# Kernel tuning notes

Measured on AMD Instinct MI355X. Metric: run time of the kernel, lower is better.

The kernel has to match this reference:

```python
import jax, jax.numpy as jnp
import numpy as np

B, LQ, LK, E, H, TOPK = 8, 512, 2048, 512, 8, 20
HD = E // H  # head dim = 64


def setup_inputs() -> dict:
    key = jax.random.key(0)
    ks = jax.random.split(key, 8)
    s = 1.0 / np.sqrt(E)
    return {
        "q": jax.random.normal(ks[0], (B, LQ, E), jnp.float32),
        "k": jax.random.normal(ks[1], (B, LK, E), jnp.float32),
        "v": jax.random.normal(ks[2], (B, LK, E), jnp.float32),
        "Wq": jax.random.normal(ks[3], (E, E), jnp.float32) * s,
        "Wk": jax.random.normal(ks[4], (E, E), jnp.float32) * s,
        "Wv": jax.random.normal(ks[5], (E, E), jnp.float32) * s,
        "Wo": jax.random.normal(ks[6], (E, E), jnp.float32) * s,
        "bo": jnp.zeros((E,), jnp.float32),
    }


def reference(q, k, v, Wq, Wk, Wv, Wo, bo):
    # torch Linear: y = x @ W^T
    def heads(x, W, L):
        return (x @ W.T).reshape(B, L, H, HD).transpose(0, 2, 1, 3)  # [B,H,L,HD]

    query = heads(q, Wq, LQ)
    key_ = heads(k, Wk, LK)
    value = heads(v, Wv, LK)

    scores = jnp.einsum("bhqd,bhkd->bhqk", query, key_) / np.sqrt(HD)
    scores = jax.nn.softmax(scores, axis=-1)  # [B,H,LQ,LK]

    topk_vals, topk_idx = jax.lax.top_k(scores, TOPK)  # [B,H,LQ,K]

    # scatter top-k probs back into a sparse weight matrix (rest zero)
    bi = jnp.arange(B)[:, None, None, None]
    hi = jnp.arange(H)[None, :, None, None]
    qi = jnp.arange(LQ)[None, None, :, None]
    attn = jnp.zeros_like(scores).at[bi, hi, qi, topk_idx].set(topk_vals)

    out = jnp.einsum("bhqk,bhkd->bhqd", attn, value)
    out = out.transpose(0, 2, 1, 3).reshape(B, LQ, E)
    return out @ Wo.T + bo + q
```

## Files before the change

kernel.cpp:

```cpp
#include <hip/hip_runtime.h>
#include <hip/hip_bf16.h>

#define NB 8
#define LQ 512
#define LK 2048
#define EE 512
#define NH 8
#define HD 64
#define NTOPK 20
#define GRP 4

typedef float f4v __attribute__((ext_vector_type(4)));
typedef short s8v __attribute__((ext_vector_type(8)));
typedef __bf16 bfrag __attribute__((ext_vector_type(8)));

__device__ inline short f2bf(float f) {
    union { float f; unsigned u; } x; x.f = f;
    unsigned r = (x.u + 0x7FFFu + ((x.u >> 16) & 1u)) >> 16;
    return (short)r;
}
__device__ inline float bf2f(short s) {
    union { unsigned u; float f; } x;
    x.u = ((unsigned)(unsigned short)s) << 16;
    return x.f;
}

__global__ __launch_bounds__(256) void cvt_all(
    const float* __restrict__ q, const float* __restrict__ k, const float* __restrict__ v,
    const float* __restrict__ wq, const float* __restrict__ wk, const float* __restrict__ wv,
    const float* __restrict__ wo,
    short* __restrict__ qb, short* __restrict__ kb, short* __restrict__ vb,
    short* __restrict__ wqb, short* __restrict__ wkb, short* __restrict__ wvb,
    short* __restrict__ wob)
{
    const float* src; short* dst; int n;
    switch (blockIdx.y) {
        case 0: src = q;  dst = qb;  n = NB * LQ * EE; break;
        case 1: src = k;  dst = kb;  n = NB * LK * EE; break;
        case 2: src = v;  dst = vb;  n = NB * LK * EE; break;
        case 3: src = wq; dst = wqb; n = EE * EE; break;
        case 4: src = wk; dst = wkb; n = EE * EE; break;
        case 5: src = wv; dst = wvb; n = EE * EE; break;
        default: src = wo; dst = wob; n = EE * EE; break;
    }
    const int nv = n >> 3;
    for (int i = blockIdx.x * 256 + threadIdx.x; i < nv; i += gridDim.x * 256) {
        f4v a = *(const f4v*)&src[(size_t)i * 8];
        f4v b = *(const f4v*)&src[(size_t)i * 8 + 4];
        s8v o;
        o[0] = f2bf(a[0]); o[1] = f2bf(a[1]); o[2] = f2bf(a[2]); o[3] = f2bf(a[3]);
        o[4] = f2bf(b[0]); o[5] = f2bf(b[1]); o[6] = f2bf(b[2]); o[7] = f2bf(b[3]);
        *(s8v*)&dst[(size_t)i * 8] = o;
    }
}

template<int MODE>
__global__ __launch_bounds__(256) void gemm_bf16(
    const short* __restrict__ A, const short* __restrict__ W,
    void* __restrict__ C, const float* __restrict__ bias,
    const float* __restrict__ resid)
{
    __shared__ short As[128][72];
    __shared__ short Bs[128][72];
    const int tid  = threadIdx.x;
    const int lane = tid & 63;
    const int wr   = (tid >> 7) & 1;
    const int wc   = (tid >> 6) & 1;
    const size_t bm = (size_t)blockIdx.y * 128;
    const int    bn = blockIdx.x * 128;

    f4v acc[4][4] = {};
    const int lr  = lane & 15;
    const int kg  = (lane >> 4) * 8;
    const int srow = tid >> 3;
    const int sc8  = (tid & 7) * 8;

    for (int ks = 0; ks < EE; ks += 64) {
        #pragma unroll
        for (int i = 0; i < 4; i++) {
            const int row = i * 32 + srow;
            *(s8v*)&As[row][sc8] = *(const s8v*)&A[(bm + row) * EE + ks + sc8];
            *(s8v*)&Bs[row][sc8] = *(const s8v*)&W[(size_t)(bn + row) * EE + ks + sc8];
        }
        __syncthreads();
        #pragma unroll
        for (int kk = 0; kk < 64; kk += 32) {
            bfrag af[4], bf[4];
            #pragma unroll
            for (int mi = 0; mi < 4; mi++)
                af[mi] = *(const bfrag*)&As[wr * 64 + mi * 16 + lr][kk + kg];
            #pragma unroll
            for (int ni = 0; ni < 4; ni++)
                bf[ni] = *(const bfrag*)&Bs[wc * 64 + ni * 16 + lr][kk + kg];
            #pragma unroll
            for (int mi = 0; mi < 4; mi++)
                #pragma unroll
                for (int ni = 0; ni < 4; ni++)
                    acc[mi][ni] = __builtin_amdgcn_mfma_f32_16x16x32_bf16(
                        af[mi], bf[ni], acc[mi][ni], 0, 0, 0);
        }
        __syncthreads();
    }

    const int rj = (lane >> 4) * 4;
    #pragma unroll
    for (int mi = 0; mi < 4; mi++) {
        #pragma unroll
        for (int ni = 0; ni < 4; ni++) {
            const int    col  = bn + wc * 64 + ni * 16 + lr;
            const size_t row0 = bm + wr * 64 + mi * 16 + rj;
            #pragma unroll
            for (int j = 0; j < 4; j++) {
                const float  v   = acc[mi][ni][j];
                const size_t idx = (row0 + j) * EE + col;
                if (MODE == 0) ((short*)C)[idx] = f2bf(v);
                else           ((float*)C)[idx] = v + bias[col] + resid[idx];
            }
        }
    }
}

__global__ __launch_bounds__(256) void score_gemm(
    const short* __restrict__ Qp, const short* __restrict__ Kp,
    short* __restrict__ Sg, int group)
{
    __shared__ short As[128][72];
    __shared__ short Bs[128][72];
    const int tid  = threadIdx.x;
    const int lane = tid & 63;
    const int wr   = (tid >> 7) & 1;
    const int wc   = (tid >> 6) & 1;
    const int z  = blockIdx.z;
    const int h  = z & 7;
    const int b  = group * GRP + (z >> 3);
    const int bm = blockIdx.y * 128;
    const int bn = blockIdx.x * 128;

    const short* Ab = Qp + (size_t)b * LQ * EE + h * HD;
    const short* Bb = Kp + (size_t)b * LK * EE + h * HD;

    #pragma unroll
    for (int i = 0; i < 4; i++) {
        const int row = i * 32 + (tid >> 3);
        const int c8  = (tid & 7) * 8;
        *(s8v*)&As[row][c8] = *(const s8v*)&Ab[(size_t)(bm + row) * EE + c8];
        *(s8v*)&Bs[row][c8] = *(const s8v*)&Bb[(size_t)(bn + row) * EE + c8];
    }
    __syncthreads();

    f4v acc[4][4] = {};
    const int lr = lane & 15;
    const int kg = (lane >> 4) * 8;
    #pragma unroll
    for (int kk = 0; kk < HD; kk += 32) {
        bfrag af[4], bf[4];
        #pragma unroll
        for (int mi = 0; mi < 4; mi++)
            af[mi] = *(const bfrag*)&As[wr * 64 + mi * 16 + lr][kk + kg];
        #pragma unroll
        for (int ni = 0; ni < 4; ni++)
            bf[ni] = *(const bfrag*)&Bs[wc * 64 + ni * 16 + lr][kk + kg];
        #pragma unroll
        for (int mi = 0; mi < 4; mi++)
            #pragma unroll
            for (int ni = 0; ni < 4; ni++)
                acc[mi][ni] = __builtin_amdgcn_mfma_f32_16x16x32_bf16(
                    af[mi], bf[ni], acc[mi][ni], 0, 0, 0);
    }

    short* Sh = Sg + (size_t)z * LQ * LK;
    const int rj = (lane >> 4) * 4;
    #pragma unroll
    for (int mi = 0; mi < 4; mi++) {
        #pragma unroll
        for (int ni = 0; ni < 4; ni++) {
            const int col = bn + wc * 64 + ni * 16 + lr;
            const int r0  = bm + wr * 64 + mi * 16 + rj;
            #pragma unroll
            for (int j = 0; j < 4; j++)
                Sh[(size_t)(r0 + j) * LK + col] = f2bf(acc[mi][ni][j] * 0.125f);
        }
    }
}

__global__ __launch_bounds__(256) void topk_pv(
    const unsigned short* __restrict__ Sg, const short* __restrict__ Vp,
    short* __restrict__ attn, int group)
{
    const int lane = threadIdx.x & 63;
    const int wid  = threadIdx.x >> 6;
    const int r  = blockIdx.x * 4 + wid;
    const int h  = (r >> 9) & 7;
    const int qi = r & 511;
    const int b  = group * GRP + (r >> 12);
    const unsigned short* Srow = Sg + (size_t)r * LK;

    s8v raw[4];
    unsigned key[32];
    const unsigned invl = 2047u - (unsigned)(lane * 8);
    #pragma unroll
    for (int t = 0; t < 4; t++) {
        raw[t] = *(const s8v*)&Srow[t * 512 + lane * 8];
        #pragma unroll
        for (int e = 0; e < 8; e++) {
            const unsigned u = (unsigned short)raw[t][e];
            const unsigned sgn = (unsigned)((int)(u << 16) >> 31);
            const unsigned mono = u ^ (0x8000u | (sgn & 0x7FFFu));
            key[t * 8 + e] = (mono << 11) | (invl - (unsigned)(t * 512 + e));
        }
    }

    unsigned v1 = 0, v2 = 0;
    #pragma unroll
    for (int c = 0; c < 32; c++) {
        const unsigned kc = key[c];
        const unsigned mn = v1 < kc ? v1 : kc;
        v2 = v2 > mn ? v2 : mn;
        v1 = v1 > kc ? v1 : kc;
    }

    unsigned K = v1;
    #pragma unroll
    for (int o = 32; o; o >>= 1) {
        const unsigned ok = __shfl_xor(K, o);
        K = K > ok ? K : ok;
    }
    const unsigned mtop = K >> 11;
    const unsigned mbits = (mtop & 0x8000u) ? (mtop ^ 0x8000u) : (~mtop & 0xFFFFu);
    union { unsigned u; float f; } mu; mu.u = mbits << 16;
    const float M = mu.f;

    float sum = 0.f;
    #pragma unroll
    for (int t = 0; t < 4; t++)
        #pragma unroll
        for (int e = 0; e < 8; e++)
            sum += __expf(bf2f(raw[t][e]) - M);
    #pragma unroll
    for (int o = 32; o; o >>= 1) sum += __shfl_xor(sum, o);
    const float inv = 1.f / sum;

    float oacc = 0.f;
    unsigned rm = 0;
    const short* Vb = Vp + (size_t)b * LK * EE + h * HD + lane;

    #pragma unroll 1
    for (int kk = 0; kk < NTOPK; kk++) {
        const unsigned idx = 2047u - (K & 2047u);
        const unsigned mo  = K >> 11;
        const unsigned sb  = (mo & 0x8000u) ? (mo ^ 0x8000u) : (~mo & 0xFFFFu);
        union { unsigned u; float f; } su; su.u = sb << 16;
        const float p = __expf(su.f - M) * inv;
        oacc += p * bf2f(Vb[(size_t)idx * EE]);

        const bool mine = (v1 == K);
        if (mine) {
            const unsigned slot = ((idx >> 9) << 3) | (idx & 7u);
            rm |= (1u << slot);
            v1 = v2;
            v2 = 0;
        }
        if (__any(v1 == 0u)) {
            if (v1 == 0u) {
                unsigned a1 = 0, a2 = 0;
                #pragma unroll
                for (int c = 0; c < 32; c++) {
                    const unsigned kc = (rm & (1u << c)) ? 0u : key[c];
                    const unsigned mn = a1 < kc ? a1 : kc;
                    a2 = a2 > mn ? a2 : mn;
                    a1 = a1 > kc ? a1 : kc;
                }
                v1 = a1; v2 = a2;
            }
        }
        K = v1;
        #pragma unroll
        for (int o = 32; o; o >>= 1) {
            const unsigned ok = __shfl_xor(K, o);
            K = K > ok ? K : ok;
        }
    }
    attn[((size_t)b * LQ + qi) * EE + h * HD + lane] = f2bf(oacc);
}

extern "C" void kernel_launch(void* const* d_in, const int* in_sizes, int n_in,
                              void* d_out, int out_size, void* d_ws, size_t ws_size,
                              hipStream_t stream)
{
    const float* q  = (const float*)d_in[0];
    const float* k  = (const float*)d_in[1];
    const float* v  = (const float*)d_in[2];
    const float* Wq = (const float*)d_in[3];
    const float* Wk = (const float*)d_in[4];
    const float* Wv = (const float*)d_in[5];
    const float* Wo = (const float*)d_in[6];
    const float* bo = (const float*)d_in[7];

    if (ws_size < ((size_t)160 << 20)) return;

    char*  ws  = (char*)d_ws;
    short* qb  = (short*)(ws);
    short* kb  = (short*)(ws + ((size_t)4   << 20));
    short* vb  = (short*)(ws + ((size_t)20  << 20));
    short* wqb = (short*)(ws + ((size_t)36  << 20));
    short* wkb = (short*)(ws + ((size_t)36  << 20) + (512 << 10));
    short* wvb = (short*)(ws + ((size_t)37  << 20));
    short* wob = (short*)(ws + ((size_t)37  << 20) + (512 << 10));
    short* Qp  = (short*)(ws + ((size_t)38  << 20));
    short* Kp  = (short*)(ws + ((size_t)42  << 20));
    short* Vp  = (short*)(ws + ((size_t)58  << 20));
    short* att = (short*)(ws + ((size_t)74  << 20));
    short* Sg  = (short*)(ws + ((size_t)80  << 20));

    dim3 blk(256);
    cvt_all<<<dim3(512, 7), blk, 0, stream>>>(q, k, v, Wq, Wk, Wv, Wo,
                                              qb, kb, vb, wqb, wkb, wvb, wob);

    gemm_bf16<0><<<dim3(4, 32),  blk, 0, stream>>>(qb, wqb, Qp, nullptr, nullptr);
    gemm_bf16<0><<<dim3(4, 128), blk, 0, stream>>>(kb, wkb, Kp, nullptr, nullptr);
    gemm_bf16<0><<<dim3(4, 128), blk, 0, stream>>>(vb, wvb, Vp, nullptr, nullptr);

    for (int g = 0; g < NB / GRP; g++) {
        score_gemm<<<dim3(LK / 128, LQ / 128, GRP * NH), blk, 0, stream>>>(Qp, Kp, Sg, g);
        topk_pv<<<dim3(GRP * NH * LQ / 4), blk, 0, stream>>>((const unsigned short*)Sg, Vp, att, g);
    }

    gemm_bf16<2><<<dim3(4, 32), blk, 0, stream>>>(att, wob, (float*)d_out, bo, q);
}
```

Before: 316.5 us.

## Process all batches in one launch and decouple top-k selection from V gathers

Makes the score GEMM and top-k kernels cover all 8 batches in a single launch each instead of two groups, which doubles the score buffer in the workspace. Replaces the shuffle-based wave reductions with DPP-based max and sum reductions. Stops storing the 32 per-lane keys in registers and recomputes them from the raw bf16 scores when a lane needs a refill, which lowers register pressure. The top-k loop now writes the selected probabilities and indices to shared memory, and the V gathers run afterwards in a fully unrolled loop, so the serial selection chain no longer waits on dependent global loads.

New measurement: 290.3 us. 8.3% less time.

```diff
diff --git a/kernel.cpp b/kernel.cpp
--- a/kernel.cpp
+++ b/kernel.cpp
@@ -8,7 +8,7 @@
 #define NH 8
 #define HD 64
 #define NTOPK 20
-#define GRP 4
+#define GRP 8
 
 typedef float f4v __attribute__((ext_vector_type(4)));
 typedef short s8v __attribute__((ext_vector_type(8)));
@@ -23,6 +23,29 @@
     union { unsigned u; float f; } x;
     x.u = ((unsigned)(unsigned short)s) << 16;
     return x.f;
+}
+
+__device__ inline unsigned wave_max_u32(unsigned x) {
+    unsigned t;
+    t = (unsigned)__builtin_amdgcn_update_dpp(0, (int)x, 0x111, 0xf, 0xf, true); x = x > t ? x : t;
+    t = (unsigned)__builtin_amdgcn_update_dpp(0, (int)x, 0x112, 0xf, 0xf, true); x = x > t ? x : t;
+    t = (unsigned)__builtin_amdgcn_update_dpp(0, (int)x, 0x114, 0xf, 0xf, true); x = x > t ? x : t;
+    t = (unsigned)__builtin_amdgcn_update_dpp(0, (int)x, 0x118, 0xf, 0xf, true); x = x > t ? x : t;
+    t = (unsigned)__builtin_amdgcn_update_dpp(0, (int)x, 0x142, 0xf, 0xf, true); x = x > t ? x : t;
+    t = (unsigned)__builtin_amdgcn_update_dpp(0, (int)x, 0x143, 0xf, 0xf, true); x = x > t ? x : t;
+    return (unsigned)__builtin_amdgcn_readlane((int)x, 63);
+}
+__device__ inline float wave_sum_f32(float x) {
+    union fi { float f; int i; } a, t;
+    a.f = x;
+    t.i = __builtin_amdgcn_update_dpp(0, a.i, 0x111, 0xf, 0xf, true); a.f += t.f;
+    t.i = __builtin_amdgcn_update_dpp(0, a.i, 0x112, 0xf, 0xf, true); a.f += t.f;
+    t.i = __builtin_amdgcn_update_dpp(0, a.i, 0x114, 0xf, 0xf, true); a.f += t.f;
+    t.i = __builtin_amdgcn_update_dpp(0, a.i, 0x118, 0xf, 0xf, true); a.f += t.f;
+    t.i = __builtin_amdgcn_update_dpp(0, a.i, 0x142, 0xf, 0xf, true); a.f += t.f;
+    t.i = __builtin_amdgcn_update_dpp(0, a.i, 0x143, 0xf, 0xf, true); a.f += t.f;
+    a.i = __builtin_amdgcn_readlane(a.i, 63);
+    return a.f;
 }
 
 __global__ __launch_bounds__(256) void cvt_all(
@@ -122,7 +145,7 @@
 
 __global__ __launch_bounds__(256) void score_gemm(
     const short* __restrict__ Qp, const short* __restrict__ Kp,
-    short* __restrict__ Sg, int group)
+    short* __restrict__ Sg)
 {
     __shared__ short As[128][72];
     __shared__ short Bs[128][72];
@@ -132,7 +155,7 @@
     const int wc   = (tid >> 6) & 1;
     const int z  = blockIdx.z;
     const int h  = z & 7;
-    const int b  = group * GRP + (z >> 3);
+    const int b  = z >> 3;
     const int bm = blockIdx.y * 128;
     const int bn = blockIdx.x * 128;
 
@@ -185,101 +208,102 @@
 
 __global__ __launch_bounds__(256) void topk_pv(
     const unsigned short* __restrict__ Sg, const short* __restrict__ Vp,
-    short* __restrict__ attn, int group)
-{
+    short* __restrict__ attn)
+{
+    __shared__ float    wp[4][NTOPK];
+    __shared__ unsigned widx[4][NTOPK];
     const int lane = threadIdx.x & 63;
     const int wid  = threadIdx.x >> 6;
     const int r  = blockIdx.x * 4 + wid;
     const int h  = (r >> 9) & 7;
     const int qi = r & 511;
-    const int b  = group * GRP + (r >> 12);
+    const int b  = r >> 12;
     const unsigned short* Srow = Sg + (size_t)r * LK;
 
     s8v raw[4];
-    unsigned key[32];
+    #pragma unroll
+    for (int t = 0; t < 4; t++)
+        raw[t] = *(const s8v*)&Srow[t * 512 + lane * 8];
+
     const unsigned invl = 2047u - (unsigned)(lane * 8);
+    unsigned v1 = 0, v2 = 0;
     #pragma unroll
     for (int t = 0; t < 4; t++) {
-        raw[t] = *(const s8v*)&Srow[t * 512 + lane * 8];
         #pragma unroll
         for (int e = 0; e < 8; e++) {
-            const unsigned u = (unsigned short)raw[t][e];
+            const unsigned u   = (unsigned short)raw[t][e];
             const unsigned sgn = (unsigned)((int)(u << 16) >> 31);
-            const unsigned mono = u ^ (0x8000u | (sgn & 0x7FFFu));
-            key[t * 8 + e] = (mono << 11) | (invl - (unsigned)(t * 512 + e));
-        }
-    }
-
-    unsigned v1 = 0, v2 = 0;
-    #pragma unroll
-    for (int c = 0; c < 32; c++) {
-        const unsigned kc = key[c];
-        const unsigned mn = v1 < kc ? v1 : kc;
-        v2 = v2 > mn ? v2 : mn;
-        v1 = v1 > kc ? v1 : kc;
-    }
-
-    unsigned K = v1;
-    #pragma unroll
-    for (int o = 32; o; o >>= 1) {
-        const unsigned ok = __shfl_xor(K, o);
-        K = K > ok ? K : ok;
-    }
-    const unsigned mtop = K >> 11;
-    const unsigned mbits = (mtop & 0x8000u) ? (mtop ^ 0x8000u) : (~mtop & 0xFFFFu);
-    union { unsigned u; float f; } mu; mu.u = mbits << 16;
-    const float M = mu.f;
-
-    float sum = 0.f;
-    #pragma unroll
-    for (int t = 0; t < 4; t++)
-        #pragma unroll
-        for (int e = 0; e < 8; e++)
-            sum += __expf(bf2f(raw[t][e]) - M);
-    #pragma unroll
-    for (int o = 32; o; o >>= 1) sum += __shfl_xor(sum, o);
-    const float inv = 1.f / sum;
+            const unsigned kc  = ((u ^ (0x8000u | (sgn & 0x7FFFu))) << 11)
+                               | (invl - (unsigned)(t * 512 + e));
+            const unsigned mn = v1 < kc ? v1 : kc;
+            v2 = v2 > mn ? v2 : mn;
+            v1 = v1 > kc ? v1 : kc;
+        }
+    }
+
+    unsigned K = wave_max_u32(v1);
+    {
+        const unsigned mtop  = K >> 11;
+        const unsigned mbits = (mtop & 0x8000u) ? (mtop ^ 0x8000u) : (~mtop & 0xFFFFu);
+        union { unsigned u; float f; } mu; mu.u = mbits << 16;
+        const float M = mu.f;
+
+        float sum = 0.f;
+        #pragma unroll
+        for (int t = 0; t < 4; t++)
+            #pragma unroll
+            for (int e = 0; e < 8; e++)
+                sum += __expf(bf2f(raw[t][e]) - M);
+        sum = wave_sum_f32(sum);
+        const float inv = 1.f / sum;
+
+        unsigned rm = 0;
+        #pragma unroll 1
+        for (int kk = 0; kk < NTOPK; kk++) {
+            const unsigned idx = 2047u - (K & 2047u);
+            const unsigned mo  = K >> 11;
+            const unsigned sb  = (mo & 0x8000u) ? (mo ^ 0x8000u) : (~mo & 0xFFFFu);
+            union { unsigned u; float f; } su; su.u = sb << 16;
+            if (lane == 0) {
+                wp[wid][kk]   = __expf(su.f - M) * inv;
+                widx[wid][kk] = idx;
+            }
+            if (v1 == K) {
+                const unsigned slot = ((idx >> 9) << 3) | (idx & 7u);
+                rm |= (1u << slot);
+                v1 = v2; v2 = 0;
+            }
+            if (__any(v1 == 0u)) {
+                if (v1 == 0u) {
+                    unsigned a1 = 0, a2 = 0;
+                    #pragma unroll
+                    for (int t = 0; t < 4; t++) {
+                        #pragma unroll
+                        for (int e = 0; e < 8; e++) {
+                            const int c = t * 8 + e;
+                            const unsigned u   = (unsigned short)raw[t][e];
+                            const unsigned sgn = (unsigned)((int)(u << 16) >> 31);
+                            unsigned kc = ((u ^ (0x8000u | (sgn & 0x7FFFu))) << 11)
+                                        | (invl - (unsigned)(t * 512 + e));
+                            kc = ((rm >> c) & 1u) ? 0u : kc;
+                            const unsigned mn = a1 < kc ? a1 : kc;
+                            a2 = a2 > mn ? a2 : mn;
+                            a1 = a1 > kc ? a1 : kc;
+                        }
+                    }
+                    v1 = a1; v2 = a2;
+                }
+            }
+            K = wave_max_u32(v1);
+        }
+    }
 
     float oacc = 0.f;
-    unsigned rm = 0;
     const short* Vb = Vp + (size_t)b * LK * EE + h * HD + lane;
-
-    #pragma unroll 1
-    for (int kk = 0; kk < NTOPK; kk++) {
-        const unsigned idx = 2047u - (K & 2047u);
-        const unsigned mo  = K >> 11;
-        const unsigned sb  = (mo & 0x8000u) ? (mo ^ 0x8000u) : (~mo & 0xFFFFu);
-        union { unsigned u; float f; } su; su.u = sb << 16;
-        const float p = __expf(su.f - M) * inv;
-        oacc += p * bf2f(Vb[(size_t)idx * EE]);
-
-        const bool mine = (v1 == K);
-        if (mine) {
-            const unsigned slot = ((idx >> 9) << 3) | (idx & 7u);
-            rm |= (1u << slot);
-            v1 = v2;
-            v2 = 0;
-        }
-        if (__any(v1 == 0u)) {
-            if (v1 == 0u) {
-                unsigned a1 = 0, a2 = 0;
-                #pragma unroll
-                for (int c = 0; c < 32; c++) {
-                    const unsigned kc = (rm & (1u << c)) ? 0u : key[c];
-                    const unsigned mn = a1 < kc ? a1 : kc;
-                    a2 = a2 > mn ? a2 : mn;
-                    a1 = a1 > kc ? a1 : kc;
-                }
-                v1 = a1; v2 = a2;
-            }
-        }
-        K = v1;
-        #pragma unroll
-        for (int o = 32; o; o >>= 1) {
-            const unsigned ok = __shfl_xor(K, o);
-            K = K > ok ? K : ok;
-        }
-    }
+    #pragma unroll
+    for (int kk = 0; kk < NTOPK; kk++)
+        oacc += wp[wid][kk] * bf2f(Vb[(size_t)widx[wid][kk] * EE]);
+
     attn[((size_t)b * LQ + qi) * EE + h * HD + lane] = f2bf(oacc);
 }
 
@@ -296,7 +320,7 @@
     const float* Wo = (const float*)d_in[6];
     const float* bo = (const float*)d_in[7];
 
-    if (ws_size < ((size_t)160 << 20)) return;
+    if (ws_size < ((size_t)208 << 20)) return;
 
     char*  ws  = (char*)d_ws;
     short* qb  = (short*)(ws);
@@ -320,10 +344,8 @@
     gemm_bf16<0><<<dim3(4, 128), blk, 0, stream>>>(kb, wkb, Kp, nullptr, nullptr);
     gemm_bf16<0><<<dim3(4, 128), blk, 0, stream>>>(vb, wvb, Vp, nullptr, nullptr);
 
-    for (int g = 0; g < NB / GRP; g++) {
-        score_gemm<<<dim3(LK / 128, LQ / 128, GRP * NH), blk, 0, stream>>>(Qp, Kp, Sg, g);
-        topk_pv<<<dim3(GRP * NH * LQ / 4), blk, 0, stream>>>((const unsigned short*)Sg, Vp, att, g);
-    }
+    score_gemm<<<dim3(LK / 128, LQ / 128, NB * NH), blk, 0, stream>>>(Qp, Kp, Sg);
+    topk_pv<<<dim3(NB * NH * LQ / 4), blk, 0, stream>>>((const unsigned short*)Sg, Vp, att);
 
     gemm_bf16<2><<<dim3(4, 32), blk, 0, stream>>>(att, wob, (float*)d_out, bo, q);
 }
```
